# Kernel optimization log

Measured on AMD Instinct MI355X. Metric: run time of the kernel, lower is better.

The kernel has to match this reference:

```python
import jax, jax.numpy as jnp
import numpy as np

N = 50000
E = 600000
D = 128
BN_EPS = 1e-5
GIN_EPS = 0.0  # init_eps=0, not learned


def setup_inputs() -> dict:
    key = jax.random.key(0)
    ks = jax.random.split(key, 8)
    x = jax.random.normal(ks[0], (N, D), dtype=jnp.float32)
    edge_index = jax.random.randint(ks[1], (2, E), 0, N, dtype=jnp.int64)
    s = 1.0 / np.sqrt(D)
    w1 = jax.random.uniform(ks[2], (D, D), jnp.float32, -s, s)
    b1 = jax.random.uniform(ks[3], (D,), jnp.float32, -s, s)
    w2 = jax.random.uniform(ks[4], (D, D), jnp.float32, -s, s)
    b2 = jax.random.uniform(ks[5], (D,), jnp.float32, -s, s)
    gamma = jnp.ones((D,), jnp.float32)
    beta = jnp.zeros((D,), jnp.float32)
    return {"x": x, "edge_index": edge_index, "w1": w1, "b1": b1,
            "w2": w2, "b2": b2, "gamma": gamma, "beta": beta}


def reference(x, edge_index, w1, b1, w2, b2, gamma, beta):
    src, dst = edge_index[0], edge_index[1]
    # GINConv sum aggregation: out[i] = sum_{(j,i) in E} x[j]
    agg = jax.ops.segment_sum(x[src], dst, num_segments=N)  # [N, D]
    h = (1.0 + GIN_EPS) * x + agg
    # 2-layer MLP (Linear-ReLU-Linear)
    h = jax.nn.relu(h @ w1 + b1)
    h = h @ w2 + b2
    # training-mode BatchNorm over nodes (biased variance)
    mean = jnp.mean(h, axis=0)
    var = jnp.var(h, axis=0)
    h = (h - mean) * jax.lax.rsqrt(var + BN_EPS) * gamma + beta
    h = jax.nn.relu(h)
    # residual (in_dim == out_dim); dropout p=0.0 -> identity
    return x + h
```

## Files before the change

### kernel.cpp

```cpp
#include <hip/hip_runtime.h>

#define NN 50000
#define EE 600000
#define DD 128
#define MAXDEG 64
#define NSLICE 32
#define EPT 8
#define RST 136
#define UNITS (NN / 16)

typedef __attribute__((ext_vector_type(8))) short short8;
typedef __attribute__((ext_vector_type(4))) float f32x4;

static __device__ __forceinline__ unsigned short f2bf(float f) {
    unsigned int u = __float_as_uint(f);
    u += 0x7FFF + ((u >> 16) & 1);
    return (unsigned short)(u >> 16);
}
static __device__ __forceinline__ float bflo(unsigned int u) {
    return __uint_as_float(u << 16);
}
static __device__ __forceinline__ float bfhi(unsigned int u) {
    return __uint_as_float(u & 0xFFFF0000u);
}

static __device__ __forceinline__ void gemm16(unsigned short* tile,
                                              const unsigned short* __restrict__ W,
                                              const float* __restrict__ bias,
                                              unsigned short* __restrict__ h2b,
                                              float* __restrict__ priv,
                                              int lane, int base, int relu, int unit) {
    int m = lane & 15, quad = lane >> 4;
    short8 af[4];
    #pragma unroll
    for (int kc = 0; kc < 4; ++kc)
        af[kc] = *(const short8*)&tile[m * RST + kc * 32 + quad * 8];
    f32x4 acc[8];
    #pragma unroll
    for (int i = 0; i < 8; ++i) acc[i] = (f32x4)0.f;

    #pragma unroll
    for (int h = 0; h < 2; ++h) {
        short8 wf[4][4];
        #pragma unroll
        for (int nt = 0; nt < 4; ++nt)
            #pragma unroll
            for (int kc = 0; kc < 4; ++kc)
                wf[nt][kc] = *(const short8*)&W[(h * 64 + nt * 16 + m) * 128 + kc * 32 + quad * 8];
        #pragma unroll
        for (int kc = 0; kc < 4; ++kc)
            #pragma unroll
            for (int nt = 0; nt < 4; ++nt)
                acc[h * 4 + nt] = __builtin_amdgcn_mfma_f32_16x16x32_bf16(af[kc], wf[nt][kc], acc[h * 4 + nt], 0, 0, 0);
    }

    if (relu) {
        #pragma unroll
        for (int nt = 0; nt < 8; ++nt) {
            int col = nt * 16 + m;
            float bv = bias[col];
            #pragma unroll
            for (int r = 0; r < 4; ++r)
                tile[(quad * 4 + r) * RST + col] = f2bf(fmaxf(acc[nt][r] + bv, 0.f));
        }
    } else {
        float* myslice = priv + (unit & (NSLICE - 1)) * 2 * DD;
        #pragma unroll
        for (int nt = 0; nt < 8; ++nt) {
            int col = nt * 16 + m;
            float bv = bias[col];
            float s = 0.f, sq = 0.f;
            #pragma unroll
            for (int r = 0; r < 4; ++r) {
                float v = acc[nt][r] + bv;
                h2b[(base + quad * 4 + r) * 128 + col] = f2bf(v);
                s += v;
                sq += v * v;
            }
            s  += __shfl_down(s, 32, 64);  sq += __shfl_down(sq, 32, 64);
            s  += __shfl_down(s, 16, 64);  sq += __shfl_down(sq, 16, 64);
            if (quad == 0) {
                atomicAdd(&myslice[col], s);
                atomicAdd(&myslice[DD + col], sq);
            }
        }
    }
}


__global__ __launch_bounds__(256) void k_prep(const float* __restrict__ w1,
                                              const float* __restrict__ w2,
                                              const float* __restrict__ x,
                                              const int* __restrict__ ei,
                                              int* __restrict__ cursor,
                                              unsigned short* __restrict__ srcPad,
                                              unsigned short* __restrict__ wt,
                                              unsigned int* __restrict__ xb) {
    int tid = blockIdx.x * 256 + threadIdx.x;
    if (tid < EE / EPT) {
        #pragma unroll
        for (int i = 0; i < EPT; ++i) {
            int e = tid + i * (EE / EPT);
            int s = ei[e];
            int d = ei[EE + e];
            int pos = atomicAdd(&cursor[d], 1);
            if (pos < MAXDEG) srcPad[(d << 6) + pos] = (unsigned short)s;
        }
    }
    if (tid < 32768) {
        int w = tid >> 14, idx = tid & 16383;
        int k = idx >> 7, n = idx & 127;
        const float* src = w ? w2 : w1;
        wt[w * 16384 + n * 128 + k] = f2bf(src[k * 128 + n]);
    }
    int xi = tid - 32768;
    if (xi >= 0 && xi < NN * DD / 4) {
        float4 v = ((const float4*)x)[xi];
        uint2 p;
        p.x = (unsigned int)f2bf(v.x) | ((unsigned int)f2bf(v.y) << 16);
        p.y = (unsigned int)f2bf(v.z) | ((unsigned int)f2bf(v.w) << 16);
        ((uint2*)xb)[xi] = p;
    }
}


__global__ __launch_bounds__(256) void k_fused(const unsigned int* __restrict__ xb,
                                               const int* __restrict__ cursor,
                                               const unsigned short* __restrict__ srcPad,
                                               const unsigned short* __restrict__ wt,
                                               const float* __restrict__ b1,
                                               const float* __restrict__ b2,
                                               unsigned short* __restrict__ h2b,
                                               float* __restrict__ priv) {
    __shared__ __align__(16) unsigned short tiles[4][16 * RST];
    int wid  = threadIdx.x >> 6;
    int lane = threadIdx.x & 63;
    int unit = blockIdx.x * 4 + wid;
    if (unit >= UNITS) return;
    unsigned short* tile = tiles[wid];
    int base = unit * 16;

    #pragma unroll
    for (int half = 0; half < 2; ++half) {
        int ct8[8], sv8[8];
        unsigned int self8[8];
        #pragma unroll
        for (int i = 0; i < 8; ++i) {
            int node = base + half * 8 + i;
            ct8[i]   = cursor[node];
            sv8[i]   = srcPad[(node << 6) + lane];
            self8[i] = xb[(node << 6) + lane];
        }
        #pragma unroll
        for (int i = 0; i < 8; ++i) {
            int cnt = ct8[i] > MAXDEG ? MAXDEG : ct8[i];
            int sv = sv8[i];
            float ax = bflo(self8[i]), ay = bfhi(self8[i]);
            int j = 0;
            for (; j + 8 <= cnt; j += 8) {
                int a0 = __shfl(sv, j, 64),     a1 = __shfl(sv, j + 1, 64);
                int a2 = __shfl(sv, j + 2, 64), a3 = __shfl(sv, j + 3, 64);
                int a4 = __shfl(sv, j + 4, 64), a5 = __shfl(sv, j + 5, 64);
                int a6 = __shfl(sv, j + 6, 64), a7 = __shfl(sv, j + 7, 64);
                unsigned int u0 = xb[(a0 << 6) + lane], u1 = xb[(a1 << 6) + lane];
                unsigned int u2 = xb[(a2 << 6) + lane], u3 = xb[(a3 << 6) + lane];
                unsigned int u4 = xb[(a4 << 6) + lane], u5 = xb[(a5 << 6) + lane];
                unsigned int u6 = xb[(a6 << 6) + lane], u7 = xb[(a7 << 6) + lane];
                ax += bflo(u0) + bflo(u1) + bflo(u2) + bflo(u3)
                    + bflo(u4) + bflo(u5) + bflo(u6) + bflo(u7);
                ay += bfhi(u0) + bfhi(u1) + bfhi(u2) + bfhi(u3)
                    + bfhi(u4) + bfhi(u5) + bfhi(u6) + bfhi(u7);
            }
            for (; j + 4 <= cnt; j += 4) {
                int a0 = __shfl(sv, j, 64),     a1 = __shfl(sv, j + 1, 64);
                int a2 = __shfl(sv, j + 2, 64), a3 = __shfl(sv, j + 3, 64);
                unsigned int u0 = xb[(a0 << 6) + lane], u1 = xb[(a1 << 6) + lane];
                unsigned int u2 = xb[(a2 << 6) + lane], u3 = xb[(a3 << 6) + lane];
                ax += bflo(u0) + bflo(u1) + bflo(u2) + bflo(u3);
                ay += bfhi(u0) + bfhi(u1) + bfhi(u2) + bfhi(u3);
            }
            for (; j < cnt; ++j) {
                int s = __shfl(sv, j, 64);
                unsigned int u = xb[(s << 6) + lane];
                ax += bflo(u);
                ay += bfhi(u);
            }
            ((unsigned int*)(tile + (half * 8 + i) * RST))[lane] =
                (unsigned int)f2bf(ax) | ((unsigned int)f2bf(ay) << 16);
        }
    }
    gemm16(tile, wt,         b1, nullptr, nullptr, lane, base, 1, unit);
    gemm16(tile, wt + 16384, b2, h2b,     priv,    lane, base, 0, unit);
}


__global__ __launch_bounds__(256) void k_final(const float* __restrict__ x,
                                               const unsigned int* __restrict__ h2,
                                               float* __restrict__ out,
                                               const float* __restrict__ priv,
                                               const float* __restrict__ gamma,
                                               const float* __restrict__ beta) {
    __shared__ float ssc[DD], ssh[DD];
    int t = threadIdx.x;
    if (t < DD) {
        float s = 0.f, sq = 0.f;
        #pragma unroll
        for (int sl = 0; sl < NSLICE; ++sl) {
            s  += priv[sl * 2 * DD + t];
            sq += priv[sl * 2 * DD + DD + t];
        }
        float mean = s * (1.0f / NN);
        float var = fmaxf(sq * (1.0f / NN) - mean * mean, 0.f);
        float sc = gamma[t] * rsqrtf(var + 1e-5f);
        ssc[t] = sc;
        ssh[t] = beta[t] - mean * sc;
    }
    __syncthreads();
    #pragma unroll
    for (int u = 0; u < 4; ++u) {
        int idx = blockIdx.x * 1024 + u * 256 + t;
        if (idx >= NN * DD / 4) return;
        int c0 = (idx & 31) * 4;
        unsigned int p0 = h2[2 * idx];
        unsigned int p1 = h2[2 * idx + 1];
        float4 xv = ((const float4*)x)[idx];
        float4 o;
        o.x = xv.x + fmaxf(fmaf(bflo(p0), ssc[c0 + 0], ssh[c0 + 0]), 0.f);
        o.y = xv.y + fmaxf(fmaf(bfhi(p0), ssc[c0 + 1], ssh[c0 + 1]), 0.f);
        o.z = xv.z + fmaxf(fmaf(bflo(p1), ssc[c0 + 2], ssh[c0 + 2]), 0.f);
        o.w = xv.w + fmaxf(fmaf(bfhi(p1), ssc[c0 + 3], ssh[c0 + 3]), 0.f);
        ((float4*)out)[idx] = o;
    }
}

extern "C" void kernel_launch(void* const* d_in, const int* in_sizes, int n_in,
                              void* d_out, int out_size, void* d_ws, size_t ws_size,
                              hipStream_t stream) {
    (void)in_sizes; (void)n_in; (void)out_size; (void)ws_size;
    const float* x     = (const float*)d_in[0];
    const int*   ei    = (const int*)d_in[1];
    const float* w1    = (const float*)d_in[2];
    const float* b1    = (const float*)d_in[3];
    const float* w2    = (const float*)d_in[4];
    const float* b2    = (const float*)d_in[5];
    const float* gamma = (const float*)d_in[6];
    const float* beta  = (const float*)d_in[7];
    float* out = (float*)d_out;
    char* wsb  = (char*)d_ws;

    int*            cursor = (int*)wsb;
    float*          priv   = (float*)(wsb + 0x31000);
    unsigned short* srcPad = (unsigned short*)(wsb + 0x40000);
    unsigned int*   xb     = (unsigned int*)(wsb + 0x680000);
    unsigned int*   h2w    = (unsigned int*)(wsb + 0x2C00000);
    unsigned short* wt     = (unsigned short*)(wsb + 0x3880000);
    unsigned short* h2b    = (unsigned short*)h2w;

    (void)hipMemsetAsync(wsb, 0, 0x39000, stream);

    k_prep <<<(32768 + NN * DD / 4 + 255) / 256, 256, 0, stream>>>(w1, w2, x, ei, cursor, srcPad, wt, xb);
    k_fused<<<(UNITS + 3) / 4, 256, 0, stream>>>(xb, cursor, srcPad, wt, b1, b2, h2b, priv);
    k_final<<<(NN * DD / 4 + 1023) / 1024, 256, 0, stream>>>(x, h2w, out, priv, gamma, beta);
}
```

Baseline: 188.8 us.

## Split each 16-node unit across four waves for gather and GEMM columns

The fused kernel now assigns one 16-node unit per block instead of one per wave. Each of the four waves gathers 4 nodes and then computes 32 of the 128 output columns of both MLP layers, sharing the tile through LDS with block barriers. This gives four times more independent waves of gather parallelism and spreads the weight-fragment loads, at the cost of block-level syncs and a redundant activation-fragment load per wave. Separately, edge bucketing in the prep kernel now uses one edge per thread instead of eight per thread.

New measurement: 175.6 us. 1.08x faster.

```diff
diff --git a/kernel.cpp b/kernel.cpp
--- a/kernel.cpp
+++ b/kernel.cpp
@@ -5,7 +5,6 @@
 #define DD 128
 #define MAXDEG 64
 #define NSLICE 32
-#define EPT 8
 #define RST 136
 #define UNITS (NN / 16)
 
@@ -24,55 +23,160 @@
     return __uint_as_float(u & 0xFFFF0000u);
 }
 
-static __device__ __forceinline__ void gemm16(unsigned short* tile,
-                                              const unsigned short* __restrict__ W,
-                                              const float* __restrict__ bias,
-                                              unsigned short* __restrict__ h2b,
-                                              float* __restrict__ priv,
-                                              int lane, int base, int relu, int unit) {
+
+__global__ __launch_bounds__(256) void k_prep(const float* __restrict__ w1,
+                                              const float* __restrict__ w2,
+                                              const float* __restrict__ x,
+                                              const int* __restrict__ ei,
+                                              int* __restrict__ cursor,
+                                              unsigned short* __restrict__ srcPad,
+                                              unsigned short* __restrict__ wt,
+                                              unsigned int* __restrict__ xb) {
+    int tid = blockIdx.x * 256 + threadIdx.x;
+    if (tid < EE) {
+        int s = ei[tid];
+        int d = ei[EE + tid];
+        int pos = atomicAdd(&cursor[d], 1);
+        if (pos < MAXDEG) srcPad[(d << 6) + pos] = (unsigned short)s;
+    }
+    if (tid < 32768) {
+        int w = tid >> 14, idx = tid & 16383;
+        int k = idx >> 7, n = idx & 127;
+        const float* src = w ? w2 : w1;
+        wt[w * 16384 + n * 128 + k] = f2bf(src[k * 128 + n]);
+    }
+    int xi = tid - 32768;
+    if (xi >= 0 && xi < NN * DD / 4) {
+        float4 v = ((const float4*)x)[xi];
+        uint2 p;
+        p.x = (unsigned int)f2bf(v.x) | ((unsigned int)f2bf(v.y) << 16);
+        p.y = (unsigned int)f2bf(v.z) | ((unsigned int)f2bf(v.w) << 16);
+        ((uint2*)xb)[xi] = p;
+    }
+}
+
+
+__global__ __launch_bounds__(256) void k_fused(const unsigned int* __restrict__ xb,
+                                               const int* __restrict__ cursor,
+                                               const unsigned short* __restrict__ srcPad,
+                                               const unsigned short* __restrict__ wt,
+                                               const float* __restrict__ b1,
+                                               const float* __restrict__ b2,
+                                               unsigned short* __restrict__ h2b,
+                                               float* __restrict__ priv) {
+    __shared__ __align__(16) unsigned short tile[16 * RST];
+    int w    = threadIdx.x >> 6;
+    int lane = threadIdx.x & 63;
+    int unit = blockIdx.x;
+    int base = unit * 16;
+
+    int ct4[4], sv4[4];
+    unsigned int self4[4];
+    #pragma unroll
+    for (int i = 0; i < 4; ++i) {
+        int node = base + w * 4 + i;
+        ct4[i]   = cursor[node];
+        sv4[i]   = srcPad[(node << 6) + lane];
+        self4[i] = xb[(node << 6) + lane];
+    }
+    #pragma unroll
+    for (int i = 0; i < 4; ++i) {
+        int cnt = ct4[i] > MAXDEG ? MAXDEG : ct4[i];
+        int sv = sv4[i];
+        float ax = bflo(self4[i]), ay = bfhi(self4[i]);
+        int j = 0;
+        for (; j + 8 <= cnt; j += 8) {
+            int a0 = __shfl(sv, j, 64),     a1 = __shfl(sv, j + 1, 64);
+            int a2 = __shfl(sv, j + 2, 64), a3 = __shfl(sv, j + 3, 64);
+            int a4 = __shfl(sv, j + 4, 64), a5 = __shfl(sv, j + 5, 64);
+            int a6 = __shfl(sv, j + 6, 64), a7 = __shfl(sv, j + 7, 64);
+            unsigned int u0 = xb[(a0 << 6) + lane], u1 = xb[(a1 << 6) + lane];
+            unsigned int u2 = xb[(a2 << 6) + lane], u3 = xb[(a3 << 6) + lane];
+            unsigned int u4 = xb[(a4 << 6) + lane], u5 = xb[(a5 << 6) + lane];
+            unsigned int u6 = xb[(a6 << 6) + lane], u7 = xb[(a7 << 6) + lane];
+            ax += bflo(u0) + bflo(u1) + bflo(u2) + bflo(u3)
+                + bflo(u4) + bflo(u5) + bflo(u6) + bflo(u7);
+            ay += bfhi(u0) + bfhi(u1) + bfhi(u2) + bfhi(u3)
+                + bfhi(u4) + bfhi(u5) + bfhi(u6) + bfhi(u7);
+        }
+        for (; j + 4 <= cnt; j += 4) {
+            int a0 = __shfl(sv, j, 64),     a1 = __shfl(sv, j + 1, 64);
+            int a2 = __shfl(sv, j + 2, 64), a3 = __shfl(sv, j + 3, 64);
+            unsigned int u0 = xb[(a0 << 6) + lane], u1 = xb[(a1 << 6) + lane];
+            unsigned int u2 = xb[(a2 << 6) + lane], u3 = xb[(a3 << 6) + lane];
+            ax += bflo(u0) + bflo(u1) + bflo(u2) + bflo(u3);
+            ay += bfhi(u0) + bfhi(u1) + bfhi(u2) + bfhi(u3);
+        }
+        for (; j < cnt; ++j) {
+            int s = __shfl(sv, j, 64);
+            unsigned int u = xb[(s << 6) + lane];
+            ax += bflo(u);
+            ay += bfhi(u);
+        }
+        ((unsigned int*)(tile + (w * 4 + i) * RST))[lane] =
+            (unsigned int)f2bf(ax) | ((unsigned int)f2bf(ay) << 16);
+    }
+    __syncthreads();
+
     int m = lane & 15, quad = lane >> 4;
+
     short8 af[4];
     #pragma unroll
     for (int kc = 0; kc < 4; ++kc)
         af[kc] = *(const short8*)&tile[m * RST + kc * 32 + quad * 8];
-    f32x4 acc[8];
-    #pragma unroll
-    for (int i = 0; i < 8; ++i) acc[i] = (f32x4)0.f;
-
-    #pragma unroll
-    for (int h = 0; h < 2; ++h) {
-        short8 wf[4][4];
-        #pragma unroll
-        for (int nt = 0; nt < 4; ++nt)
+    __syncthreads();
+    {
+        short8 wf[2][4];
+        #pragma unroll
+        for (int t = 0; t < 2; ++t)
             #pragma unroll
             for (int kc = 0; kc < 4; ++kc)
-                wf[nt][kc] = *(const short8*)&W[(h * 64 + nt * 16 + m) * 128 + kc * 32 + quad * 8];
+                wf[t][kc] = *(const short8*)&wt[((w * 2 + t) * 16 + m) * 128 + kc * 32 + quad * 8];
+        f32x4 acc[2];
+        acc[0] = (f32x4)0.f; acc[1] = (f32x4)0.f;
         #pragma unroll
         for (int kc = 0; kc < 4; ++kc)
             #pragma unroll
-            for (int nt = 0; nt < 4; ++nt)
-                acc[h * 4 + nt] = __builtin_amdgcn_mfma_f32_16x16x32_bf16(af[kc], wf[nt][kc], acc[h * 4 + nt], 0, 0, 0);
-    }
-
-    if (relu) {
-        #pragma unroll
-        for (int nt = 0; nt < 8; ++nt) {
-            int col = nt * 16 + m;
-            float bv = bias[col];
+            for (int t = 0; t < 2; ++t)
+                acc[t] = __builtin_amdgcn_mfma_f32_16x16x32_bf16(af[kc], wf[t][kc], acc[t], 0, 0, 0);
+        #pragma unroll
+        for (int t = 0; t < 2; ++t) {
+            int col = (w * 2 + t) * 16 + m;
+            float bv = b1[col];
             #pragma unroll
             for (int r = 0; r < 4; ++r)
-                tile[(quad * 4 + r) * RST + col] = f2bf(fmaxf(acc[nt][r] + bv, 0.f));
-        }
-    } else {
+                tile[(quad * 4 + r) * RST + col] = f2bf(fmaxf(acc[t][r] + bv, 0.f));
+        }
+    }
+    __syncthreads();
+
+    #pragma unroll
+    for (int kc = 0; kc < 4; ++kc)
+        af[kc] = *(const short8*)&tile[m * RST + kc * 32 + quad * 8];
+    {
+        const unsigned short* W2t = wt + 16384;
+        short8 wf[2][4];
+        #pragma unroll
+        for (int t = 0; t < 2; ++t)
+            #pragma unroll
+            for (int kc = 0; kc < 4; ++kc)
+                wf[t][kc] = *(const short8*)&W2t[((w * 2 + t) * 16 + m) * 128 + kc * 32 + quad * 8];
+        f32x4 acc[2];
+        acc[0] = (f32x4)0.f; acc[1] = (f32x4)0.f;
+        #pragma unroll
+        for (int kc = 0; kc < 4; ++kc)
+            #pragma unroll
+            for (int t = 0; t < 2; ++t)
+                acc[t] = __builtin_amdgcn_mfma_f32_16x16x32_bf16(af[kc], wf[t][kc], acc[t], 0, 0, 0);
         float* myslice = priv + (unit & (NSLICE - 1)) * 2 * DD;
         #pragma unroll
-        for (int nt = 0; nt < 8; ++nt) {
-            int col = nt * 16 + m;
-            float bv = bias[col];
+        for (int t = 0; t < 2; ++t) {
+            int col = (w * 2 + t) * 16 + m;
+            float bv = b2[col];
             float s = 0.f, sq = 0.f;
             #pragma unroll
             for (int r = 0; r < 4; ++r) {
-                float v = acc[nt][r] + bv;
+                float v = acc[t][r] + bv;
                 h2b[(base + quad * 4 + r) * 128 + col] = f2bf(v);
                 s += v;
                 sq += v * v;
@@ -85,112 +189,6 @@
             }
         }
     }
-}
-
-
-__global__ __launch_bounds__(256) void k_prep(const float* __restrict__ w1,
-                                              const float* __restrict__ w2,
-                                              const float* __restrict__ x,
-                                              const int* __restrict__ ei,
-                                              int* __restrict__ cursor,
-                                              unsigned short* __restrict__ srcPad,
-                                              unsigned short* __restrict__ wt,
-                                              unsigned int* __restrict__ xb) {
-    int tid = blockIdx.x * 256 + threadIdx.x;
-    if (tid < EE / EPT) {
-        #pragma unroll
-        for (int i = 0; i < EPT; ++i) {
-            int e = tid + i * (EE / EPT);
-            int s = ei[e];
-            int d = ei[EE + e];
-            int pos = atomicAdd(&cursor[d], 1);
-            if (pos < MAXDEG) srcPad[(d << 6) + pos] = (unsigned short)s;
-        }
-    }
-    if (tid < 32768) {
-        int w = tid >> 14, idx = tid & 16383;
-        int k = idx >> 7, n = idx & 127;
-        const float* src = w ? w2 : w1;
-        wt[w * 16384 + n * 128 + k] = f2bf(src[k * 128 + n]);
-    }
-    int xi = tid - 32768;
-    if (xi >= 0 && xi < NN * DD / 4) {
-        float4 v = ((const float4*)x)[xi];
-        uint2 p;
-        p.x = (unsigned int)f2bf(v.x) | ((unsigned int)f2bf(v.y) << 16);
-        p.y = (unsigned int)f2bf(v.z) | ((unsigned int)f2bf(v.w) << 16);
-        ((uint2*)xb)[xi] = p;
-    }
-}
-
-
-__global__ __launch_bounds__(256) void k_fused(const unsigned int* __restrict__ xb,
-                                               const int* __restrict__ cursor,
-                                               const unsigned short* __restrict__ srcPad,
-                                               const unsigned short* __restrict__ wt,
-                                               const float* __restrict__ b1,
-                                               const float* __restrict__ b2,
-                                               unsigned short* __restrict__ h2b,
-                                               float* __restrict__ priv) {
-    __shared__ __align__(16) unsigned short tiles[4][16 * RST];
-    int wid  = threadIdx.x >> 6;
-    int lane = threadIdx.x & 63;
-    int unit = blockIdx.x * 4 + wid;
-    if (unit >= UNITS) return;
-    unsigned short* tile = tiles[wid];
-    int base = unit * 16;
-
-    #pragma unroll
-    for (int half = 0; half < 2; ++half) {
-        int ct8[8], sv8[8];
-        unsigned int self8[8];
-        #pragma unroll
-        for (int i = 0; i < 8; ++i) {
-            int node = base + half * 8 + i;
-            ct8[i]   = cursor[node];
-            sv8[i]   = srcPad[(node << 6) + lane];
-            self8[i] = xb[(node << 6) + lane];
-        }
-        #pragma unroll
-        for (int i = 0; i < 8; ++i) {
-            int cnt = ct8[i] > MAXDEG ? MAXDEG : ct8[i];
-            int sv = sv8[i];
-            float ax = bflo(self8[i]), ay = bfhi(self8[i]);
-            int j = 0;
-            for (; j + 8 <= cnt; j += 8) {
-                int a0 = __shfl(sv, j, 64),     a1 = __shfl(sv, j + 1, 64);
-                int a2 = __shfl(sv, j + 2, 64), a3 = __shfl(sv, j + 3, 64);
-                int a4 = __shfl(sv, j + 4, 64), a5 = __shfl(sv, j + 5, 64);
-                int a6 = __shfl(sv, j + 6, 64), a7 = __shfl(sv, j + 7, 64);
-                unsigned int u0 = xb[(a0 << 6) + lane], u1 = xb[(a1 << 6) + lane];
-                unsigned int u2 = xb[(a2 << 6) + lane], u3 = xb[(a3 << 6) + lane];
-                unsigned int u4 = xb[(a4 << 6) + lane], u5 = xb[(a5 << 6) + lane];
-                unsigned int u6 = xb[(a6 << 6) + lane], u7 = xb[(a7 << 6) + lane];
-                ax += bflo(u0) + bflo(u1) + bflo(u2) + bflo(u3)
-                    + bflo(u4) + bflo(u5) + bflo(u6) + bflo(u7);
-                ay += bfhi(u0) + bfhi(u1) + bfhi(u2) + bfhi(u3)
-                    + bfhi(u4) + bfhi(u5) + bfhi(u6) + bfhi(u7);
-            }
-            for (; j + 4 <= cnt; j += 4) {
-                int a0 = __shfl(sv, j, 64),     a1 = __shfl(sv, j + 1, 64);
-                int a2 = __shfl(sv, j + 2, 64), a3 = __shfl(sv, j + 3, 64);
-                unsigned int u0 = xb[(a0 << 6) + lane], u1 = xb[(a1 << 6) + lane];
-                unsigned int u2 = xb[(a2 << 6) + lane], u3 = xb[(a3 << 6) + lane];
-                ax += bflo(u0) + bflo(u1) + bflo(u2) + bflo(u3);
-                ay += bfhi(u0) + bfhi(u1) + bfhi(u2) + bfhi(u3);
-            }
-            for (; j < cnt; ++j) {
-                int s = __shfl(sv, j, 64);
-                unsigned int u = xb[(s << 6) + lane];
-                ax += bflo(u);
-                ay += bfhi(u);
-            }
-            ((unsigned int*)(tile + (half * 8 + i) * RST))[lane] =
-                (unsigned int)f2bf(ax) | ((unsigned int)f2bf(ay) << 16);
-        }
-    }
-    gemm16(tile, wt,         b1, nullptr, nullptr, lane, base, 1, unit);
-    gemm16(tile, wt + 16384, b2, h2b,     priv,    lane, base, 0, unit);
 }
 
 
@@ -259,6 +257,6 @@
     (void)hipMemsetAsync(wsb, 0, 0x39000, stream);
 
     k_prep <<<(32768 + NN * DD / 4 + 255) / 256, 256, 0, stream>>>(w1, w2, x, ei, cursor, srcPad, wt, xb);
-    k_fused<<<(UNITS + 3) / 4, 256, 0, stream>>>(xb, cursor, srcPad, wt, b1, b2, h2b, priv);
+    k_fused<<<UNITS, 256, 0, stream>>>(xb, cursor, srcPad, wt, b1, b2, h2b, priv);
     k_final<<<(NN * DD / 4 + 1023) / 1024, 256, 0, stream>>>(x, h2w, out, priv, gamma, beta);
 }
```
